# Kernel optimization log

Hardware: AMD Instinct MI355X
Metric: run time of the kernel (lower is better)

Reference implementation:

```python
import jax, jax.numpy as jnp
import numpy as np

NUM_HEADS = 16
SIZE_PER_HEAD = 64
HIDDEN = NUM_HEADS * SIZE_PER_HEAD  # 1024
B, F, T = 4, 1024, 1024
NEG_INF = -10000.0


def setup_inputs() -> dict:
    key = jax.random.key(0)
    ks = jax.random.split(key, 6)
    scale = 0.02
    return {
        "from_tensor": jax.random.normal(ks[0], (B, F, HIDDEN), dtype=jnp.float32),
        "to_tensor": jax.random.normal(ks[1], (B, T, HIDDEN), dtype=jnp.float32),
        "attention_mask": jnp.ones((B, F, T), dtype=jnp.float32),
        "Wq": jax.random.normal(ks[2], (HIDDEN, HIDDEN), dtype=jnp.float32) * scale,
        "bq": jnp.zeros((HIDDEN,), dtype=jnp.float32),
        "Wk": jax.random.normal(ks[3], (HIDDEN, HIDDEN), dtype=jnp.float32) * scale,
        "bk": jnp.zeros((HIDDEN,), dtype=jnp.float32),
        "Wv": jax.random.normal(ks[4], (HIDDEN, HIDDEN), dtype=jnp.float32) * scale,
        "bv": jnp.zeros((HIDDEN,), dtype=jnp.float32),
    }


def _split_heads(x, seq_len):
    # [B, S, H*Dh] -> [B, H, S, Dh]
    return x.reshape(B, seq_len, NUM_HEADS, SIZE_PER_HEAD).transpose(0, 2, 1, 3)


def reference(from_tensor, to_tensor, attention_mask, Wq, bq, Wk, bk, Wv, bv):
    # Q/K/V dense projections (query_act/key_act/value_act are None -> linear)
    q = _split_heads(from_tensor @ Wq + bq, F)   # [B,H,F,Dh]
    k = _split_heads(to_tensor @ Wk + bk, T)     # [B,H,T,Dh]
    v = _split_heads(to_tensor @ Wv + bv, T)     # [B,H,T,Dh]

    # scaled dot-product attention scores: [B,H,F,T]
    scores = jnp.einsum("bhfd,bhtd->bhft", q, k) / jnp.sqrt(
        jnp.asarray(SIZE_PER_HEAD, dtype=q.dtype))

    # BERT-style mask adder: mask==1 -> attend, mask==0 -> -10000
    adder = (1.0 - attention_mask[:, None, :, :]) * NEG_INF
    scores = scores + adder

    attention_probs = jax.nn.softmax(scores, axis=-1)  # dropout_prob=0.0

    ctx = jnp.einsum("bhft,bhtd->bhfd", attention_probs, v)  # [B,H,F,Dh]
    ctx = ctx.transpose(0, 2, 1, 3).reshape(B, F, NUM_HEADS * SIZE_PER_HEAD)
    return ctx, attention_probs
```

## Files before the change

### kernel.cpp

```cpp
#include <hip/hip_runtime.h>

typedef unsigned short u16;
typedef __bf16 bf16x8 __attribute__((ext_vector_type(8)));
typedef float f32x4 __attribute__((ext_vector_type(4)));
typedef u16 u16x8 __attribute__((ext_vector_type(8)));
typedef u16 u16x4 __attribute__((ext_vector_type(4)));

#define NUM_HEADS 16
#define HIDDEN 1024
#define BATCH 4
#define SEQ 1024
#define C1 0.1803368809109783f
#define LOG2E 1.4426950408889634f

#define VMCNT0 asm volatile("s_waitcnt vmcnt(0)" ::: "memory")

static __device__ __forceinline__ u16 f2bf(float x) {
  unsigned u = __float_as_uint(x);
  u = u + 0x7FFFu + ((u >> 16) & 1u);
  return (u16)(u >> 16);
}
static __device__ __forceinline__ float bf2f(u16 b) {
  return __uint_as_float(((unsigned)b) << 16);
}
static __device__ __forceinline__ void async16(u16* lds, const u16* g) {
  __builtin_amdgcn_global_load_lds(
      (const __attribute__((address_space(1))) void*)g,
      (__attribute__((address_space(3))) void*)lds, 16, 0, 0);
}

__global__ __launch_bounds__(256) void k_prep(
    const float* __restrict__ from, u16* __restrict__ Af,
    const float* __restrict__ to, u16* __restrict__ At,
    const float* __restrict__ Wq, const float* __restrict__ Wk,
    const float* __restrict__ Wv, u16* __restrict__ Wt,
    const float* __restrict__ mask, u16* __restrict__ adder, int* __restrict__ flags) {
  int bid = blockIdx.x;
  int tid = threadIdx.x;
  if (bid < 4096) {
    const float* in = (bid < 2048) ? from : to;
    u16* out = (bid < 2048) ? Af : At;
    int i = (bid & 2047) * 256 + tid;
    float4 a = ((const float4*)in)[i * 2];
    float4 b = ((const float4*)in)[i * 2 + 1];
    u16x8 v;
    v[0] = f2bf(a.x); v[1] = f2bf(a.y); v[2] = f2bf(a.z); v[3] = f2bf(a.w);
    v[4] = f2bf(b.x); v[5] = f2bf(b.y); v[6] = f2bf(b.z); v[7] = f2bf(b.w);
    *(u16x8*)&out[(size_t)i * 8] = v;
  } else if (bid < 4864) {
    __shared__ float tile[64][65];
    int wid = bid - 4096;
    int z = wid >> 8, rem = wid & 255;
    int x = rem & 15, y = rem >> 4;
    const float* W = (z == 0) ? Wq : (z == 1) ? Wk : Wv;
    u16* out = Wt + (size_t)z * HIDDEN * HIDDEN;
    int k0 = y * 64, n0 = x * 64;
    int r = tid >> 6, c = tid & 63;
#pragma unroll
    for (int i = 0; i < 16; ++i)
      tile[i * 4 + r][c] = W[(size_t)(k0 + i * 4 + r) * HIDDEN + n0 + c];
    __syncthreads();
#pragma unroll
    for (int i = 0; i < 16; ++i)
      out[(size_t)(n0 + i * 4 + r) * HIDDEN + k0 + c] = f2bf(tile[c][i * 4 + r]);
  } else {
    int wid = bid - 4864;
    int tt = wid & 7, ft = (wid >> 3) & 7, b = wid >> 6;
    __shared__ int sflag;
    if (tid == 0) sflag = 0;
    __syncthreads();
    size_t base = ((size_t)b * SEQ + ft * 128) * SEQ + tt * 128;
    int any = 0;
#pragma unroll
    for (int i = 0; i < 16; ++i) {
      int idx = i * 256 + tid;
      int r = idx >> 5, c4 = idx & 31;
      float4 v = *(const float4*)&mask[base + (size_t)r * SEQ + c4 * 4];
      any |= (v.x != 1.0f) | (v.y != 1.0f) | (v.z != 1.0f) | (v.w != 1.0f);
    }
    if (any) sflag = 1;
    __syncthreads();
    if (sflag) {
#pragma unroll
      for (int i = 0; i < 16; ++i) {
        int idx = i * 256 + tid;
        int r = idx >> 5, c4 = idx & 31;
        float4 v = *(const float4*)&mask[base + (size_t)r * SEQ + c4 * 4];
        u16x4 o;
        o[0] = f2bf((1.0f - v.x) * -10000.0f * LOG2E);
        o[1] = f2bf((1.0f - v.y) * -10000.0f * LOG2E);
        o[2] = f2bf((1.0f - v.z) * -10000.0f * LOG2E);
        o[3] = f2bf((1.0f - v.w) * -10000.0f * LOG2E);
        *(u16x4*)&adder[base + (size_t)r * SEQ + c4 * 4] = o;
      }
    }
    if (tid == 0) flags[(b * 8 + ft) * 8 + tt] = sflag;
  }
}

__global__ __launch_bounds__(256) void k_gemm(
    const u16* __restrict__ Af, const u16* __restrict__ At,
    const u16* __restrict__ Wt,
    const float* __restrict__ bq, const float* __restrict__ bk, const float* __restrict__ bv,
    u16* __restrict__ Qh, u16* __restrict__ Kh, u16* __restrict__ Vt) {
  __shared__ u16 sAB[2 * 128 * 64];
  u16* sA = sAB;
  u16* sB = sAB + 128 * 64;
  int which = blockIdx.z;
  const u16* A = (which == 0) ? Af : At;
  const u16* B = Wt + (size_t)which * HIDDEN * HIDDEN;
  const float* bias = (which == 0) ? bq : (which == 1) ? bk : bv;
  int wg = blockIdx.x + 8 * blockIdx.y;
  int xcd = wg & 7, j = wg >> 3;
  int ntile = j & 7, mstrip = xcd * 4 + (j >> 3);
  int m0 = mstrip * 128, n0 = ntile * 128;
  int tid = threadIdx.x, w = tid >> 6, lane = tid & 63;
  int wr = w >> 1, wc = w & 1;
  int g = lane >> 4, cc = lane & 15;

  f32x4 acc[4][4] = {};

  int sx[4], srow[4], scol[4];
#pragma unroll
  for (int i = 0; i < 4; ++i) {
    int ch = w * 4 + i;
    int x = ch * 1024 + lane * 16;
    int row = x >> 7;
    int colb = (x & 127) ^ ((row & 7) << 4);
    sx[i] = ch * 512;
    srow[i] = row;
    scol[i] = colb >> 1;
  }

  for (int kt = 0; kt < HIDDEN / 64; ++kt) {
    __syncthreads();
#pragma unroll
    for (int i = 0; i < 4; ++i) {
      async16(&sA[sx[i]], A + (size_t)(m0 + srow[i]) * HIDDEN + kt * 64 + scol[i]);
      async16(&sB[sx[i]], B + (size_t)(n0 + srow[i]) * HIDDEN + kt * 64 + scol[i]);
    }
    VMCNT0;
    __syncthreads();
#pragma unroll
    for (int kk = 0; kk < 2; ++kk) {
      bf16x8 af[4], bfr[4];
#pragma unroll
      for (int mf = 0; mf < 4; ++mf) {
        int row = wr * 64 + mf * 16 + cc;
        int colb = (kk * 64 + (g << 4)) ^ ((row & 7) << 4);
        af[mf] = *(const bf16x8*)&sA[(row * 128 + colb) >> 1];
      }
#pragma unroll
      for (int nf = 0; nf < 4; ++nf) {
        int row = wc * 64 + nf * 16 + cc;
        int colb = (kk * 64 + (g << 4)) ^ ((row & 7) << 4);
        bfr[nf] = *(const bf16x8*)&sB[(row * 128 + colb) >> 1];
      }
#pragma unroll
      for (int mf = 0; mf < 4; ++mf)
#pragma unroll
        for (int nf = 0; nf < 4; ++nf)
          acc[mf][nf] = __builtin_amdgcn_mfma_f32_16x16x32_bf16(af[mf], bfr[nf], acc[mf][nf], 0, 0, 0);
    }
  }

  if (which != 2) {
#pragma unroll
    for (int mf = 0; mf < 4; ++mf) {
#pragma unroll
      for (int nf = 0; nf < 4; ++nf) {
        int n = n0 + wc * 64 + nf * 16 + cc;
        float bval = bias[n];
        int h = n >> 6, d = n & 63;
#pragma unroll
        for (int r = 0; r < 4; ++r) {
          int m = m0 + wr * 64 + mf * 16 + g * 4 + r;
          int b = m >> 10, s = m & 1023;
          u16 o = f2bf(acc[mf][nf][r] + bval);
          if (which == 0)
            Qh[((((size_t)b * NUM_HEADS + h) * SEQ + s) << 6) + d] = o;
          else
            Kh[((((size_t)b * NUM_HEADS + h) * SEQ + s) << 6) + d] = o;
        }
      }
    }
  } else {
    __syncthreads();
    char* T = (char*)sAB;
#pragma unroll
    for (int mf = 0; mf < 4; ++mf) {
#pragma unroll
      for (int nf = 0; nf < 4; ++nf) {
        int nl = wc * 64 + nf * 16 + cc;
        float bval = bias[n0 + nl];
        int mlb = wr * 64 + mf * 16 + g * 4;
        u16x4 v;
#pragma unroll
        for (int r = 0; r < 4; ++r) v[r] = f2bf(acc[mf][nf][r] + bval);
        int byte = nl * 256 + ((mlb * 2) ^ ((nl & 7) << 4));
        *(u16x4*)(T + byte) = v;
      }
    }
    __syncthreads();
    int nl = tid >> 1, mh = (tid & 1) * 64;
    int b = m0 >> 10, s0 = m0 & 1023;
    u16* dst = &Vt[((size_t)b * 1024 + n0 + nl) * SEQ + s0 + mh];
#pragma unroll
    for (int j2 = 0; j2 < 8; ++j2) {
      int byte = nl * 256 + (((mh + j2 * 8) * 2) ^ ((nl & 7) << 4));
      *(u16x8*)&dst[j2 * 8] = *(const u16x8*)(T + byte);
    }
  }
}

__global__ __launch_bounds__(256, 3) void k_attn1(
    const u16* __restrict__ Qh, const u16* __restrict__ Kh,
    const u16* __restrict__ adder, const int* __restrict__ flags,
    float* __restrict__ invl) {
  __shared__ u16 sQ[128 * 64];
  __shared__ u16 sK[128 * 64];
  int ft = blockIdx.x, h = blockIdx.y, b = blockIdx.z;
  int f0 = ft * 128;
  int bh = b * NUM_HEADS + h;
  const u16* Qg = Qh + ((size_t)bh * SEQ + f0) * 64;
  const u16* Kg = Kh + (size_t)bh * SEQ * 64;
  int tid = threadIdx.x, w = tid >> 6, lane = tid & 63;
  int g = lane >> 4, cc = lane & 15;
  const int fbase = w * 32;

  int flgmask = 0;
#pragma unroll
  for (int tt = 0; tt < 8; ++tt)
    flgmask |= (flags[(b * 8 + ft) * 8 + tt] != 0) << tt;

  int sx[4], srow7[4], scol7[4];
#pragma unroll
  for (int i = 0; i < 4; ++i) {
    int ch = w * 4 + i;
    int x = ch * 1024 + lane * 16;
    sx[i] = ch * 512;
    int r7 = x >> 7;
    int c7 = (x & 127) ^ ((r7 & 7) << 4);
    srow7[i] = r7; scol7[i] = c7 >> 1;
  }

#pragma unroll
  for (int i = 0; i < 4; ++i)
    async16(&sQ[sx[i]], Qg + (size_t)srow7[i] * 64 + scol7[i]);

  float l_run[8];
#pragma unroll
  for (int i = 0; i < 8; ++i) l_run[i] = 0.0f;

  for (int tt = 0; tt < 8; ++tt) {
    __syncthreads();
#pragma unroll
    for (int i = 0; i < 4; ++i)
      async16(&sK[sx[i]], Kg + (size_t)(tt * 128 + srow7[i]) * 64 + scol7[i]);
    VMCNT0;
    __syncthreads();

    f32x4 s[2][8] = {};
#pragma unroll
    for (int kk = 0; kk < 2; ++kk) {
      bf16x8 aq[2], bk8[8];
#pragma unroll
      for (int mf = 0; mf < 2; ++mf) {
        int row = fbase + mf * 16 + cc;
        int colb = (kk * 64 + (g << 4)) ^ ((row & 7) << 4);
        aq[mf] = *(const bf16x8*)&sQ[(row * 128 + colb) >> 1];
      }
#pragma unroll
      for (int nf = 0; nf < 8; ++nf) {
        int row = nf * 16 + cc;
        int colb = (kk * 64 + (g << 4)) ^ ((row & 7) << 4);
        bk8[nf] = *(const bf16x8*)&sK[(row * 128 + colb) >> 1];
      }
#pragma unroll
      for (int mf = 0; mf < 2; ++mf)
#pragma unroll
        for (int nf = 0; nf < 8; ++nf)
          s[mf][nf] = __builtin_amdgcn_mfma_f32_16x16x32_bf16(aq[mf], bk8[nf], s[mf][nf], 0, 0, 0);
    }
#pragma unroll
    for (int mf = 0; mf < 2; ++mf)
#pragma unroll
      for (int nf = 0; nf < 8; ++nf)
        s[mf][nf] = s[mf][nf] * C1;
    if ((flgmask >> tt) & 1) {
      for (int mf = 0; mf < 2; ++mf)
        for (int nf = 0; nf < 8; ++nf)
          for (int r = 0; r < 4; ++r) {
            int frow = f0 + fbase + mf * 16 + g * 4 + r;
            int tcol = tt * 128 + nf * 16 + cc;
            s[mf][nf][r] += bf2f(adder[((size_t)b * SEQ + frow) * SEQ + tcol]);
          }
    }
#pragma unroll
    for (int mf = 0; mf < 2; ++mf)
#pragma unroll
      for (int r = 0; r < 4; ++r) {
        float sum = 0.f;
#pragma unroll
        for (int nf = 0; nf < 8; ++nf) sum += exp2f(s[mf][nf][r]);
        sum += __shfl_xor(sum, 1, 16);
        sum += __shfl_xor(sum, 2, 16);
        sum += __shfl_xor(sum, 4, 16);
        sum += __shfl_xor(sum, 8, 16);
        l_run[mf * 4 + r] += sum;
      }
  }

  if (cc == 0) {
#pragma unroll
    for (int mf = 0; mf < 2; ++mf)
#pragma unroll
      for (int r = 0; r < 4; ++r)
        invl[(size_t)bh * SEQ + f0 + fbase + mf * 16 + g * 4 + r] =
            1.0f / l_run[mf * 4 + r];
  }
}

__global__ __launch_bounds__(256) void k_attn2(
    const u16* __restrict__ Qh, const u16* __restrict__ Kh, const u16* __restrict__ Vt,
    const u16* __restrict__ adder, const int* __restrict__ flags,
    const float* __restrict__ invl,
    float* __restrict__ ctx, float* __restrict__ probs) {
  __shared__ u16 sQ[128 * 64];
  __shared__ u16 sK[128 * 64];
  __shared__ u16 sV[64 * 128];
  __shared__ u16 sP[128 * 128];
  int ft = blockIdx.x, h = blockIdx.y, b = blockIdx.z;
  int f0 = ft * 128;
  int bh = b * NUM_HEADS + h;
  const u16* Qg = Qh + ((size_t)bh * SEQ + f0) * 64;
  const u16* Kg = Kh + (size_t)bh * SEQ * 64;
  const u16* Vg = Vt + (size_t)bh * 64 * SEQ;
  int tid = threadIdx.x, w = tid >> 6, lane = tid & 63;
  int g = lane >> 4, cc = lane & 15;
  const int fbase = w * 32;

  int flgmask = 0;
#pragma unroll
  for (int tt = 0; tt < 8; ++tt)
    flgmask |= (flags[(b * 8 + ft) * 8 + tt] != 0) << tt;

  int sx[4], srow7[4], scol7[4], srow8[4], scol8[4];
#pragma unroll
  for (int i = 0; i < 4; ++i) {
    int ch = w * 4 + i;
    int x = ch * 1024 + lane * 16;
    sx[i] = ch * 512;
    int r7 = x >> 7;
    int c7 = (x & 127) ^ ((r7 & 7) << 4);
    srow7[i] = r7; scol7[i] = c7 >> 1;
    int r8 = x >> 8;
    int c8 = (x & 255) ^ ((r8 & 7) << 4);
    srow8[i] = r8; scol8[i] = c8 >> 1;
  }

#pragma unroll
  for (int i = 0; i < 4; ++i)
    async16(&sQ[sx[i]], Qg + (size_t)srow7[i] * 64 + scol7[i]);

  float inv_l[8];
#pragma unroll
  for (int mf = 0; mf < 2; ++mf)
#pragma unroll
    for (int r = 0; r < 4; ++r)
      inv_l[mf * 4 + r] =
          invl[(size_t)bh * SEQ + f0 + fbase + mf * 16 + g * 4 + r];

  f32x4 accO[2][4] = {};

  for (int tt = 0; tt < 8; ++tt) {
    __syncthreads();
#pragma unroll
    for (int i = 0; i < 4; ++i) {
      async16(&sK[sx[i]], Kg + (size_t)(tt * 128 + srow7[i]) * 64 + scol7[i]);
      async16(&sV[sx[i]], Vg + (size_t)srow8[i] * SEQ + tt * 128 + scol8[i]);
    }
    VMCNT0;
    __syncthreads();

    f32x4 s[2][8] = {};
#pragma unroll
    for (int kk = 0; kk < 2; ++kk) {
      bf16x8 aq[2], bk8[8];
#pragma unroll
      for (int mf = 0; mf < 2; ++mf) {
        int row = fbase + mf * 16 + cc;
        int colb = (kk * 64 + (g << 4)) ^ ((row & 7) << 4);
        aq[mf] = *(const bf16x8*)&sQ[(row * 128 + colb) >> 1];
      }
#pragma unroll
      for (int nf = 0; nf < 8; ++nf) {
        int row = nf * 16 + cc;
        int colb = (kk * 64 + (g << 4)) ^ ((row & 7) << 4);
        bk8[nf] = *(const bf16x8*)&sK[(row * 128 + colb) >> 1];
      }
#pragma unroll
      for (int mf = 0; mf < 2; ++mf)
#pragma unroll
        for (int nf = 0; nf < 8; ++nf)
          s[mf][nf] = __builtin_amdgcn_mfma_f32_16x16x32_bf16(aq[mf], bk8[nf], s[mf][nf], 0, 0, 0);
    }
#pragma unroll
    for (int mf = 0; mf < 2; ++mf)
#pragma unroll
      for (int nf = 0; nf < 8; ++nf)
        s[mf][nf] = s[mf][nf] * C1;
    if ((flgmask >> tt) & 1) {
      for (int mf = 0; mf < 2; ++mf)
        for (int nf = 0; nf < 8; ++nf)
          for (int r = 0; r < 4; ++r) {
            int frow = f0 + fbase + mf * 16 + g * 4 + r;
            int tcol = tt * 128 + nf * 16 + cc;
            s[mf][nf][r] += bf2f(adder[((size_t)b * SEQ + frow) * SEQ + tcol]);
          }
    }
#pragma unroll
    for (int mf = 0; mf < 2; ++mf)
#pragma unroll
      for (int nf = 0; nf < 8; ++nf)
#pragma unroll
        for (int r = 0; r < 4; ++r) {
          int idx = mf * 4 + r;
          float p = exp2f(s[mf][nf][r]) * inv_l[idx];
          int frow = fbase + mf * 16 + g * 4 + r;
          int tcol = nf * 16 + cc;
          probs[(((size_t)bh * SEQ) + f0 + frow) * SEQ + tt * 128 + tcol] = p;
          sP[(frow * 256 + ((tcol * 2) ^ ((frow & 7) << 4))) >> 1] = f2bf(p);
        }
#pragma unroll
    for (int ks = 0; ks < 4; ++ks) {
      bf16x8 ap[2], bv8[4];
#pragma unroll
      for (int mf = 0; mf < 2; ++mf) {
        int row = fbase + mf * 16 + cc;
        int colb = (ks * 64 + (g << 4)) ^ ((row & 7) << 4);
        ap[mf] = *(const bf16x8*)&sP[(row * 256 + colb) >> 1];
      }
#pragma unroll
      for (int nf = 0; nf < 4; ++nf) {
        int row = nf * 16 + cc;
        int colb = (ks * 64 + (g << 4)) ^ ((row & 7) << 4);
        bv8[nf] = *(const bf16x8*)&sV[(row * 256 + colb) >> 1];
      }
#pragma unroll
      for (int mf = 0; mf < 2; ++mf)
#pragma unroll
        for (int nf = 0; nf < 4; ++nf)
          accO[mf][nf] = __builtin_amdgcn_mfma_f32_16x16x32_bf16(ap[mf], bv8[nf], accO[mf][nf], 0, 0, 0);
    }
  }

#pragma unroll
  for (int mf = 0; mf < 2; ++mf)
#pragma unroll
    for (int nf = 0; nf < 4; ++nf)
#pragma unroll
      for (int r = 0; r < 4; ++r) {
        int frow = fbase + mf * 16 + g * 4 + r;
        int d = nf * 16 + cc;
        ctx[((size_t)b * SEQ + f0 + frow) * HIDDEN + h * 64 + d] = accO[mf][nf][r];
      }
}

extern "C" void kernel_launch(void* const* d_in, const int* in_sizes, int n_in,
                              void* d_out, int out_size, void* d_ws, size_t ws_size,
                              hipStream_t stream) {
  const float* from = (const float*)d_in[0];
  const float* to   = (const float*)d_in[1];
  const float* mask = (const float*)d_in[2];
  const float* Wq   = (const float*)d_in[3];
  const float* bq   = (const float*)d_in[4];
  const float* Wk   = (const float*)d_in[5];
  const float* bk   = (const float*)d_in[6];
  const float* Wv   = (const float*)d_in[7];
  const float* bv   = (const float*)d_in[8];

  char* ws = (char*)d_ws;
  u16* Af    = (u16*)(ws);
  u16* At    = (u16*)(ws + 8388608);
  u16* Wt    = (u16*)(ws + 16777216);
  u16* adder = (u16*)(ws + 23068672);
  int* flags = (int*)(ws + 31457280);
  u16* Qh    = (u16*)(ws + 31458304);
  u16* Kh    = (u16*)(ws + 39846912);
  u16* Vt    = (u16*)(ws + 48235520);
  float* invl = (float*)(ws);

  float* ctx = (float*)d_out;
  float* probs = ctx + (size_t)BATCH * SEQ * HIDDEN;

  k_prep<<<5120, 256, 0, stream>>>(from, Af, to, At, Wq, Wk, Wv, Wt, mask, adder, flags);
  k_gemm<<<dim3(8, 32, 3), 256, 0, stream>>>(Af, At, Wt, bq, bk, bv, Qh, Kh, Vt);
  k_attn1<<<dim3(8, 16, 4), 256, 0, stream>>>(Qh, Kh, adder, flags, invl);
  k_attn2<<<dim3(8, 16, 4), 256, 0, stream>>>(Qh, Kh, Vt, adder, flags, invl, ctx, probs);
}
```

Baseline: 205.0 us.

## Stage probs and ctx stores through LDS for vectorized nontemporal writes; load two K tiles

```diff
diff --git a/kernel.cpp b/kernel.cpp
--- a/kernel.cpp
+++ b/kernel.cpp
@@ -27,6 +27,9 @@
   __builtin_amdgcn_global_load_lds(
       (const __attribute__((address_space(1))) void*)g,
       (__attribute__((address_space(3))) void*)lds, 16, 0, 0);
+}
+static __device__ __forceinline__ void ntstore4(float* p, f32x4 v) {
+  __builtin_nontemporal_store(v, (f32x4*)p);
 }
 
 __global__ __launch_bounds__(256) void k_prep(
@@ -218,7 +221,7 @@
     const u16* __restrict__ adder, const int* __restrict__ flags,
     float* __restrict__ invl) {
   __shared__ u16 sQ[128 * 64];
-  __shared__ u16 sK[128 * 64];
+  __shared__ u16 sK[2][128 * 64];
   int ft = blockIdx.x, h = blockIdx.y, b = blockIdx.z;
   int f0 = ft * 128;
   int bh = b * NUM_HEADS + h;
@@ -252,63 +255,69 @@
 #pragma unroll
   for (int i = 0; i < 8; ++i) l_run[i] = 0.0f;
 
-  for (int tt = 0; tt < 8; ++tt) {
-    __syncthreads();
-#pragma unroll
-    for (int i = 0; i < 4; ++i)
-      async16(&sK[sx[i]], Kg + (size_t)(tt * 128 + srow7[i]) * 64 + scol7[i]);
+  for (int tt4 = 0; tt4 < 4; ++tt4) {
+    __syncthreads();
+#pragma unroll
+    for (int i = 0; i < 4; ++i) {
+      async16(&sK[0][sx[i]], Kg + (size_t)(tt4 * 256 + srow7[i]) * 64 + scol7[i]);
+      async16(&sK[1][sx[i]], Kg + (size_t)(tt4 * 256 + 128 + srow7[i]) * 64 + scol7[i]);
+    }
     VMCNT0;
     __syncthreads();
 
-    f32x4 s[2][8] = {};
-#pragma unroll
-    for (int kk = 0; kk < 2; ++kk) {
-      bf16x8 aq[2], bk8[8];
-#pragma unroll
-      for (int mf = 0; mf < 2; ++mf) {
-        int row = fbase + mf * 16 + cc;
-        int colb = (kk * 64 + (g << 4)) ^ ((row & 7) << 4);
-        aq[mf] = *(const bf16x8*)&sQ[(row * 128 + colb) >> 1];
-      }
-#pragma unroll
-      for (int nf = 0; nf < 8; ++nf) {
-        int row = nf * 16 + cc;
-        int colb = (kk * 64 + (g << 4)) ^ ((row & 7) << 4);
-        bk8[nf] = *(const bf16x8*)&sK[(row * 128 + colb) >> 1];
+#pragma unroll
+    for (int half = 0; half < 2; ++half) {
+      int tt = tt4 * 2 + half;
+      f32x4 s[2][8] = {};
+#pragma unroll
+      for (int kk = 0; kk < 2; ++kk) {
+        bf16x8 aq[2], bk8[8];
+#pragma unroll
+        for (int mf = 0; mf < 2; ++mf) {
+          int row = fbase + mf * 16 + cc;
+          int colb = (kk * 64 + (g << 4)) ^ ((row & 7) << 4);
+          aq[mf] = *(const bf16x8*)&sQ[(row * 128 + colb) >> 1];
+        }
+#pragma unroll
+        for (int nf = 0; nf < 8; ++nf) {
+          int row = nf * 16 + cc;
+          int colb = (kk * 64 + (g << 4)) ^ ((row & 7) << 4);
+          bk8[nf] = *(const bf16x8*)&sK[half][(row * 128 + colb) >> 1];
+        }
+#pragma unroll
+        for (int mf = 0; mf < 2; ++mf)
+#pragma unroll
+          for (int nf = 0; nf < 8; ++nf)
+            s[mf][nf] = __builtin_amdgcn_mfma_f32_16x16x32_bf16(aq[mf], bk8[nf], s[mf][nf], 0, 0, 0);
       }
 #pragma unroll
       for (int mf = 0; mf < 2; ++mf)
 #pragma unroll
         for (int nf = 0; nf < 8; ++nf)
-          s[mf][nf] = __builtin_amdgcn_mfma_f32_16x16x32_bf16(aq[mf], bk8[nf], s[mf][nf], 0, 0, 0);
-    }
-#pragma unroll
-    for (int mf = 0; mf < 2; ++mf)
-#pragma unroll
-      for (int nf = 0; nf < 8; ++nf)
-        s[mf][nf] = s[mf][nf] * C1;
-    if ((flgmask >> tt) & 1) {
+          s[mf][nf] = s[mf][nf] * C1;
+      if ((flgmask >> tt) & 1) {
+        for (int mf = 0; mf < 2; ++mf)
+          for (int nf = 0; nf < 8; ++nf)
+            for (int r = 0; r < 4; ++r) {
+              int frow = f0 + fbase + mf * 16 + g * 4 + r;
+              int tcol = tt * 128 + nf * 16 + cc;
+              s[mf][nf][r] += bf2f(adder[((size_t)b * SEQ + frow) * SEQ + tcol]);
+            }
+      }
+#pragma unroll
       for (int mf = 0; mf < 2; ++mf)
-        for (int nf = 0; nf < 8; ++nf)
-          for (int r = 0; r < 4; ++r) {
-            int frow = f0 + fbase + mf * 16 + g * 4 + r;
-            int tcol = tt * 128 + nf * 16 + cc;
-            s[mf][nf][r] += bf2f(adder[((size_t)b * SEQ + frow) * SEQ + tcol]);
-          }
-    }
-#pragma unroll
-    for (int mf = 0; mf < 2; ++mf)
-#pragma unroll
-      for (int r = 0; r < 4; ++r) {
-        float sum = 0.f;
-#pragma unroll
-        for (int nf = 0; nf < 8; ++nf) sum += exp2f(s[mf][nf][r]);
-        sum += __shfl_xor(sum, 1, 16);
-        sum += __shfl_xor(sum, 2, 16);
-        sum += __shfl_xor(sum, 4, 16);
-        sum += __shfl_xor(sum, 8, 16);
-        l_run[mf * 4 + r] += sum;
-      }
+#pragma unroll
+        for (int r = 0; r < 4; ++r) {
+          float sum = 0.f;
+#pragma unroll
+          for (int nf = 0; nf < 8; ++nf) sum += exp2f(s[mf][nf][r]);
+          sum += __shfl_xor(sum, 1, 16);
+          sum += __shfl_xor(sum, 2, 16);
+          sum += __shfl_xor(sum, 4, 16);
+          sum += __shfl_xor(sum, 8, 16);
+          l_run[mf * 4 + r] += sum;
+        }
+    }
   }
 
   if (cc == 0) {
@@ -429,9 +438,19 @@
           float p = exp2f(s[mf][nf][r]) * inv_l[idx];
           int frow = fbase + mf * 16 + g * 4 + r;
           int tcol = nf * 16 + cc;
-          probs[(((size_t)bh * SEQ) + f0 + frow) * SEQ + tt * 128 + tcol] = p;
           sP[(frow * 256 + ((tcol * 2) ^ ((frow & 7) << 4))) >> 1] = f2bf(p);
         }
+#pragma unroll
+    for (int sw = 0; sw < 8; ++sw) {
+      int row = fbase + sw * 4 + (lane >> 4);
+      int colb = ((lane & 15) * 16) ^ ((row & 7) << 4);
+      u16x8 pv = *(const u16x8*)&sP[(row * 256 + colb) >> 1];
+      float* dst = &probs[((size_t)bh * SEQ + f0 + row) * SEQ + tt * 128 + (lane & 15) * 8];
+      f32x4 o0 = {bf2f(pv[0]), bf2f(pv[1]), bf2f(pv[2]), bf2f(pv[3])};
+      f32x4 o1 = {bf2f(pv[4]), bf2f(pv[5]), bf2f(pv[6]), bf2f(pv[7])};
+      ntstore4(dst, o0);
+      ntstore4(dst + 4, o1);
+    }
 #pragma unroll
     for (int ks = 0; ks < 4; ++ks) {
       bf16x8 ap[2], bv8[4];
@@ -455,6 +474,8 @@
     }
   }
 
+  __syncthreads();
+  float* sPf = (float*)sP;
 #pragma unroll
   for (int mf = 0; mf < 2; ++mf)
 #pragma unroll
@@ -462,9 +483,14 @@
 #pragma unroll
       for (int r = 0; r < 4; ++r) {
         int frow = fbase + mf * 16 + g * 4 + r;
-        int d = nf * 16 + cc;
-        ctx[((size_t)b * SEQ + f0 + frow) * HIDDEN + h * 64 + d] = accO[mf][nf][r];
-      }
+        sPf[frow * 64 + nf * 16 + cc] = accO[mf][nf][r];
+      }
+#pragma unroll
+  for (int sw = 0; sw < 8; ++sw) {
+    int row = fbase + sw * 4 + (lane >> 4);
+    f32x4 v = *(const f32x4*)&sPf[row * 64 + (lane & 15) * 4];
+    ntstore4(&ctx[((size_t)b * SEQ + f0 + row) * HIDDEN + h * 64 + (lane & 15) * 4], v);
+  }
 }
 
 extern "C" void kernel_launch(void* const* d_in, const int* in_sizes, int n_in,
```

Result: slower. 241.6 us (+17.8%).

## Split QKV GEMM into Q GEMM and fused K/V GEMM sharing the A tile

Applied to the files above, without the earlier changes.

```diff
diff --git a/kernel.cpp b/kernel.cpp
--- a/kernel.cpp
+++ b/kernel.cpp
@@ -98,18 +98,13 @@
   }
 }
 
-__global__ __launch_bounds__(256) void k_gemm(
-    const u16* __restrict__ Af, const u16* __restrict__ At,
-    const u16* __restrict__ Wt,
-    const float* __restrict__ bq, const float* __restrict__ bk, const float* __restrict__ bv,
-    u16* __restrict__ Qh, u16* __restrict__ Kh, u16* __restrict__ Vt) {
-  __shared__ u16 sAB[2 * 128 * 64];
-  u16* sA = sAB;
-  u16* sB = sAB + 128 * 64;
-  int which = blockIdx.z;
-  const u16* A = (which == 0) ? Af : At;
-  const u16* B = Wt + (size_t)which * HIDDEN * HIDDEN;
-  const float* bias = (which == 0) ? bq : (which == 1) ? bk : bv;
+__global__ __launch_bounds__(256) void k_gemmQ(
+    const u16* __restrict__ Af, const u16* __restrict__ Wt,
+    const float* __restrict__ bq, u16* __restrict__ Qh) {
+  __shared__ u16 sA[128 * 64];
+  __shared__ u16 sB[128 * 64];
+  const u16* A = Af;
+  const u16* B = Wt;
   int wg = blockIdx.x + 8 * blockIdx.y;
   int xcd = wg & 7, j = wg >> 3;
   int ntile = j & 7, mstrip = xcd * 4 + (j >> 3);
@@ -164,52 +159,131 @@
     }
   }
 
-  if (which != 2) {
-#pragma unroll
-    for (int mf = 0; mf < 4; ++mf) {
+#pragma unroll
+  for (int mf = 0; mf < 4; ++mf) {
+#pragma unroll
+    for (int nf = 0; nf < 4; ++nf) {
+      int n = n0 + wc * 64 + nf * 16 + cc;
+      float bval = bq[n];
+      int h = n >> 6, d = n & 63;
+#pragma unroll
+      for (int r = 0; r < 4; ++r) {
+        int m = m0 + wr * 64 + mf * 16 + g * 4 + r;
+        int b = m >> 10, s = m & 1023;
+        Qh[((((size_t)b * NUM_HEADS + h) * SEQ + s) << 6) + d] = f2bf(acc[mf][nf][r] + bval);
+      }
+    }
+  }
+}
+
+__global__ __launch_bounds__(256) void k_gemmKV(
+    const u16* __restrict__ At, const u16* __restrict__ Wt,
+    const float* __restrict__ bk_, const float* __restrict__ bv_,
+    u16* __restrict__ Kh, u16* __restrict__ Vt) {
+  __shared__ u16 sA[128 * 64];
+  __shared__ u16 sBk[128 * 64];
+  __shared__ u16 sBv[128 * 64];
+  const u16* Bk = Wt + (size_t)1 * HIDDEN * HIDDEN;
+  const u16* Bv = Wt + (size_t)2 * HIDDEN * HIDDEN;
+  int wg = blockIdx.x + 8 * blockIdx.y;
+  int xcd = wg & 7, j = wg >> 3;
+  int ntile = j & 7, mstrip = xcd * 4 + (j >> 3);
+  int m0 = mstrip * 128, n0 = ntile * 128;
+  int tid = threadIdx.x, w = tid >> 6, lane = tid & 63;
+  int wr = w >> 1, wc = w & 1;
+  int g = lane >> 4, cc = lane & 15;
+
+  f32x4 acck[4][4] = {};
+  f32x4 accv[4][4] = {};
+
+  int sx[4], srow[4], scol[4];
+#pragma unroll
+  for (int i = 0; i < 4; ++i) {
+    int ch = w * 4 + i;
+    int x = ch * 1024 + lane * 16;
+    int row = x >> 7;
+    int colb = (x & 127) ^ ((row & 7) << 4);
+    sx[i] = ch * 512;
+    srow[i] = row;
+    scol[i] = colb >> 1;
+  }
+
+  for (int kt = 0; kt < HIDDEN / 64; ++kt) {
+    __syncthreads();
+#pragma unroll
+    for (int i = 0; i < 4; ++i) {
+      async16(&sA[sx[i]], At + (size_t)(m0 + srow[i]) * HIDDEN + kt * 64 + scol[i]);
+      async16(&sBk[sx[i]], Bk + (size_t)(n0 + srow[i]) * HIDDEN + kt * 64 + scol[i]);
+      async16(&sBv[sx[i]], Bv + (size_t)(n0 + srow[i]) * HIDDEN + kt * 64 + scol[i]);
+    }
+    VMCNT0;
+    __syncthreads();
+#pragma unroll
+    for (int kk = 0; kk < 2; ++kk) {
+      bf16x8 af[4], bkf[4], bvf[4];
+#pragma unroll
+      for (int mf = 0; mf < 4; ++mf) {
+        int row = wr * 64 + mf * 16 + cc;
+        int colb = (kk * 64 + (g << 4)) ^ ((row & 7) << 4);
+        af[mf] = *(const bf16x8*)&sA[(row * 128 + colb) >> 1];
+      }
 #pragma unroll
       for (int nf = 0; nf < 4; ++nf) {
-        int n = n0 + wc * 64 + nf * 16 + cc;
-        float bval = bias[n];
-        int h = n >> 6, d = n & 63;
-#pragma unroll
-        for (int r = 0; r < 4; ++r) {
-          int m = m0 + wr * 64 + mf * 16 + g * 4 + r;
-          int b = m >> 10, s = m & 1023;
-          u16 o = f2bf(acc[mf][nf][r] + bval);
-          if (which == 0)
-            Qh[((((size_t)b * NUM_HEADS + h) * SEQ + s) << 6) + d] = o;
-          else
-            Kh[((((size_t)b * NUM_HEADS + h) * SEQ + s) << 6) + d] = o;
+        int row = wc * 64 + nf * 16 + cc;
+        int colb = (kk * 64 + (g << 4)) ^ ((row & 7) << 4);
+        bkf[nf] = *(const bf16x8*)&sBk[(row * 128 + colb) >> 1];
+        bvf[nf] = *(const bf16x8*)&sBv[(row * 128 + colb) >> 1];
+      }
+#pragma unroll
+      for (int mf = 0; mf < 4; ++mf)
+#pragma unroll
+        for (int nf = 0; nf < 4; ++nf) {
+          acck[mf][nf] = __builtin_amdgcn_mfma_f32_16x16x32_bf16(af[mf], bkf[nf], acck[mf][nf], 0, 0, 0);
+          accv[mf][nf] = __builtin_amdgcn_mfma_f32_16x16x32_bf16(af[mf], bvf[nf], accv[mf][nf], 0, 0, 0);
         }
-      }
-    }
-  } else {
-    __syncthreads();
-    char* T = (char*)sAB;
-#pragma unroll
-    for (int mf = 0; mf < 4; ++mf) {
-#pragma unroll
-      for (int nf = 0; nf < 4; ++nf) {
-        int nl = wc * 64 + nf * 16 + cc;
-        float bval = bias[n0 + nl];
-        int mlb = wr * 64 + mf * 16 + g * 4;
-        u16x4 v;
-#pragma unroll
-        for (int r = 0; r < 4; ++r) v[r] = f2bf(acc[mf][nf][r] + bval);
-        int byte = nl * 256 + ((mlb * 2) ^ ((nl & 7) << 4));
-        *(u16x4*)(T + byte) = v;
-      }
-    }
-    __syncthreads();
-    int nl = tid >> 1, mh = (tid & 1) * 64;
-    int b = m0 >> 10, s0 = m0 & 1023;
-    u16* dst = &Vt[((size_t)b * 1024 + n0 + nl) * SEQ + s0 + mh];
-#pragma unroll
-    for (int j2 = 0; j2 < 8; ++j2) {
-      int byte = nl * 256 + (((mh + j2 * 8) * 2) ^ ((nl & 7) << 4));
-      *(u16x8*)&dst[j2 * 8] = *(const u16x8*)(T + byte);
-    }
+    }
+  }
+
+#pragma unroll
+  for (int mf = 0; mf < 4; ++mf) {
+#pragma unroll
+    for (int nf = 0; nf < 4; ++nf) {
+      int n = n0 + wc * 64 + nf * 16 + cc;
+      float bval = bk_[n];
+      int h = n >> 6, d = n & 63;
+#pragma unroll
+      for (int r = 0; r < 4; ++r) {
+        int m = m0 + wr * 64 + mf * 16 + g * 4 + r;
+        int b = m >> 10, s = m & 1023;
+        Kh[((((size_t)b * NUM_HEADS + h) * SEQ + s) << 6) + d] = f2bf(acck[mf][nf][r] + bval);
+      }
+    }
+  }
+
+  __syncthreads();
+  char* T = (char*)sA;
+#pragma unroll
+  for (int mf = 0; mf < 4; ++mf) {
+#pragma unroll
+    for (int nf = 0; nf < 4; ++nf) {
+      int nl = wc * 64 + nf * 16 + cc;
+      float bval = bv_[n0 + nl];
+      int mlb = wr * 64 + mf * 16 + g * 4;
+      u16x4 v;
+#pragma unroll
+      for (int r = 0; r < 4; ++r) v[r] = f2bf(accv[mf][nf][r] + bval);
+      int byte = nl * 256 + ((mlb * 2) ^ ((nl & 7) << 4));
+      *(u16x4*)(T + byte) = v;
+    }
+  }
+  __syncthreads();
+  int nl = tid >> 1, mh = (tid & 1) * 64;
+  int b = m0 >> 10, s0 = m0 & 1023;
+  u16* dst = &Vt[((size_t)b * 1024 + n0 + nl) * SEQ + s0 + mh];
+#pragma unroll
+  for (int j2 = 0; j2 < 8; ++j2) {
+    int byte = nl * 256 + (((mh + j2 * 8) * 2) ^ ((nl & 7) << 4));
+    *(u16x8*)&dst[j2 * 8] = *(const u16x8*)(T + byte);
   }
 }
 
@@ -495,7 +569,8 @@
   float* probs = ctx + (size_t)BATCH * SEQ * HIDDEN;
 
   k_prep<<<5120, 256, 0, stream>>>(from, Af, to, At, Wq, Wk, Wv, Wt, mask, adder, flags);
-  k_gemm<<<dim3(8, 32, 3), 256, 0, stream>>>(Af, At, Wt, bq, bk, bv, Qh, Kh, Vt);
+  k_gemmQ<<<dim3(8, 32), 256, 0, stream>>>(Af, Wt, bq, Qh);
+  k_gemmKV<<<dim3(8, 32), 256, 0, stream>>>(At, Wt, bk, bv, Kh, Vt);
   k_attn1<<<dim3(8, 16, 4), 256, 0, stream>>>(Qh, Kh, adder, flags, invl);
   k_attn2<<<dim3(8, 16, 4), 256, 0, stream>>>(Qh, Kh, Vt, adder, flags, invl, ctx, probs);
 }
```

Measured after the change: 197.9 us. -3.5%, faster.
